# Performance work log

Hardware: AMD Instinct MI355X
Metric: run time of the kernel (lower is better)

Reference implementation:

```python
import jax, jax.numpy as jnp
import numpy as np

N_HEAD, M_DIM, K_DIM, V_DIM = 16, 1024, 64, 64
LN_EPS = 1e-5


def setup_inputs() -> dict:
    key = jax.random.key(0)
    ks = jax.random.split(key, 10)
    B, L = 4, 2048
    q = jax.random.normal(ks[0], (B, L, M_DIM), dtype=jnp.float32)
    k = jax.random.normal(ks[1], (B, L, M_DIM), dtype=jnp.float32)
    v = jax.random.normal(ks[2], (B, L, M_DIM), dtype=jnp.float32)
    s = 1.0 / np.sqrt(M_DIM)
    W_qs = jax.random.normal(ks[3], (M_DIM, N_HEAD * K_DIM), dtype=jnp.float32) * s
    W_ks = jax.random.normal(ks[4], (M_DIM, N_HEAD * K_DIM), dtype=jnp.float32) * s
    W_vs = jax.random.normal(ks[5], (M_DIM, N_HEAD * V_DIM), dtype=jnp.float32) * s
    fc_w = jax.random.normal(ks[6], (N_HEAD * V_DIM, M_DIM), dtype=jnp.float32) * (1.0 / np.sqrt(N_HEAD * V_DIM))
    fc_b = jnp.zeros((M_DIM,), dtype=jnp.float32)
    ln_g = jnp.ones((M_DIM,), dtype=jnp.float32)
    ln_b = jnp.zeros((M_DIM,), dtype=jnp.float32)
    return {"q": q, "k": k, "v": v, "W_qs": W_qs, "W_ks": W_ks, "W_vs": W_vs,
            "fc_w": fc_w, "fc_b": fc_b, "ln_g": ln_g, "ln_b": ln_b}


def reference(q, k, v, W_qs, W_ks, W_vs, fc_w, fc_b, ln_g, ln_b):
    B, Lq, _ = q.shape
    residual = q
    # project and split heads: [B, L, H, D]
    qh = (q @ W_qs).reshape(B, Lq, N_HEAD, K_DIM)
    kh = (k @ W_ks).reshape(B, k.shape[1], N_HEAD, K_DIM)
    vh = (v @ W_vs).reshape(B, v.shape[1], N_HEAD, V_DIM)
    temperature = np.power(K_DIM, 0.5).astype(np.float32)
    # attention scores [B, H, Lq, Lk]
    attn = jnp.einsum('bqhd,bkhd->bhqk', qh, kh) / temperature
    attn = jax.nn.softmax(attn, axis=-1)
    out = jnp.einsum('bhqk,bkhd->bqhd', attn, vh).reshape(B, Lq, N_HEAD * V_DIM)
    out = out @ fc_w + fc_b
    x = out + residual
    mu = jnp.mean(x, axis=-1, keepdims=True)
    var = jnp.mean(jnp.square(x - mu), axis=-1, keepdims=True)
    return (x - mu) * jax.lax.rsqrt(var + LN_EPS) * ln_g + ln_b
```

## Files before the change

### kernel.cpp

```cpp
#include <hip/hip_runtime.h>
#include <math.h>

#define NHEAD 16
#define MDIM  1024
#define KD    64
#define BATCH 4
#define SEQ   2048
#define MROWS (BATCH*SEQ)

using short8 = __attribute__((ext_vector_type(8))) short;
using f4     = __attribute__((ext_vector_type(4))) float;
using f16x   = __attribute__((ext_vector_type(16))) float;

__device__ inline short f2bf(float x) {
  union { float f; unsigned u; } v; v.f = x;
  unsigned r = v.u + 0x7fffu + ((v.u >> 16) & 1u);
  return (short)(r >> 16);
}

__device__ __forceinline__ float fast_exp2(float x) {
#if __has_builtin(__builtin_amdgcn_exp2f)
  return __builtin_amdgcn_exp2f(x);
#else
  return exp2f(x);
#endif
}

__device__ __forceinline__ int pack_bf16(float lo, float hi) {
#if __has_builtin(__builtin_amdgcn_cvt_pk_bf16_f32)
  auto t = __builtin_amdgcn_cvt_pk_bf16_f32(lo, hi);
  int r; __builtin_memcpy(&r, &t, 4); return r;
#else
  unsigned u0 = __float_as_uint(lo) + 0x8000u;
  unsigned u1 = __float_as_uint(hi) + 0x8000u;
  return (int)__builtin_amdgcn_perm(u1, u0, 0x07060302u);
#endif
}

__device__ __forceinline__ void g2l16(const void* g, void* l) {
  __builtin_amdgcn_global_load_lds((const __attribute__((address_space(1))) unsigned int*)g,
                                   (__attribute__((address_space(3))) unsigned int*)l, 16, 0, 0);
}

__global__ void wtrans_kernel(const float* __restrict__ w0, const float* __restrict__ w1,
                              const float* __restrict__ w2, const float* __restrict__ w3,
                              short* __restrict__ o0, short* __restrict__ o1,
                              short* __restrict__ o2, short* __restrict__ o3) {
  int z = blockIdx.z;
  const float* in = z == 0 ? w0 : (z == 1 ? w1 : (z == 2 ? w2 : w3));
  short* out = z == 0 ? o0 : (z == 1 ? o1 : (z == 2 ? o2 : o3));
  __shared__ float t[32][33];
  int bx = blockIdx.x * 32, by = blockIdx.y * 32;
  int tx = threadIdx.x, ty = threadIdx.y;
#pragma unroll
  for (int i = 0; i < 4; i++)
    t[ty + i * 8][tx] = in[(size_t)(by + ty + i * 8) * MDIM + bx + tx];
  __syncthreads();
#pragma unroll
  for (int i = 0; i < 4; i++)
    out[(size_t)(bx + ty + i * 8) * MDIM + by + tx] = f2bf(t[tx][ty + i * 8]);
}

__global__ void cvt_kernel(const float* __restrict__ q, const float* __restrict__ k,
                           const float* __restrict__ v, short* __restrict__ qb,
                           short* __restrict__ kb, short* __restrict__ vb) {
  const float* in = blockIdx.y == 0 ? q : (blockIdx.y == 1 ? k : v);
  short* out = blockIdx.y == 0 ? qb : (blockIdx.y == 1 ? kb : vb);
  size_t i = (size_t)blockIdx.x * 256 + threadIdx.x;
  float4 a = ((const float4*)in)[2 * i];
  float4 b = ((const float4*)in)[2 * i + 1];
  short8 s = {f2bf(a.x), f2bf(a.y), f2bf(a.z), f2bf(a.w),
              f2bf(b.x), f2bf(b.y), f2bf(b.z), f2bf(b.w)};
  ((short8*)out)[i] = s;
}

#define GEMM_STAGE_SETUP(Ab, Bt)                                                   \
  int srow = lane >> 2;                                                            \
  int sch = (lane & 3) ^ (srow & 3);                                               \
  const short* aSrc0 = Ab + (size_t)(m0 + wave * 32 + srow) * 1024 + sch * 8;      \
  const short* aSrc1 = aSrc0 + (size_t)16 * 1024;                                  \
  const short* bSrc0 = Bt + (size_t)(n0 + wave * 32 + srow) * 1024 + sch * 8;      \
  const short* bSrc1 = bSrc0 + (size_t)16 * 1024;

#define GEMM_MAIN_LOOP()                                                           \
  auto stage = [&](int k0, int b) {                                                \
    g2l16(aSrc0 + k0, &As[b][wave * 1024]);                                        \
    g2l16(aSrc1 + k0, &As[b][wave * 1024 + 512]);                                  \
    g2l16(bSrc0 + k0, &Bs[b][wave * 1024]);                                        \
    g2l16(bSrc1 + k0, &Bs[b][wave * 1024 + 512]);                                  \
  };                                                                               \
  stage(0, 0);                                                                     \
  __syncthreads();                                                                 \
  int aoff = (quad ^ (low & 3)) * 8;                                               \
  for (int k0 = 0; k0 < 1024; k0 += 32) {                                          \
    int b = (k0 >> 5) & 1;                                                         \
    if (k0 + 32 < 1024) stage(k0 + 32, b ^ 1);                                     \
    short8 af[4], bfr[4];                                                          \
    _Pragma("unroll")                                                              \
    for (int m = 0; m < 4; m++) af[m] = *(const short8*)&As[b][(wr + m * 16 + low) * 32 + aoff]; \
    _Pragma("unroll")                                                              \
    for (int n = 0; n < 4; n++) bfr[n] = *(const short8*)&Bs[b][(wc + n * 16 + low) * 32 + aoff]; \
    _Pragma("unroll")                                                              \
    for (int m = 0; m < 4; m++)                                                    \
      _Pragma("unroll")                                                            \
      for (int n = 0; n < 4; n++)                                                  \
        acc[m][n] = __builtin_amdgcn_mfma_f32_16x16x32_bf16(af[m], bfr[n], acc[m][n], 0, 0, 0); \
    __syncthreads();                                                               \
  }

__launch_bounds__(256, 4)
__global__ void gemm_qkv_kernel(const short* __restrict__ qb, const short* __restrict__ kb,
                                const short* __restrict__ vb, const short* __restrict__ Wqt,
                                const short* __restrict__ Wkt, const short* __restrict__ Wvt,
                                short* __restrict__ Qh, short* __restrict__ Kh,
                                short* __restrict__ Vt) {
  __shared__ __attribute__((aligned(16))) short As[2][128 * 32];
  __shared__ __attribute__((aligned(16))) short Bs[2][128 * 32];
  int z = blockIdx.z;
  const short* Ab = z == 0 ? qb : (z == 1 ? kb : vb);
  const short* Bt = z == 0 ? Wqt : (z == 1 ? Wkt : Wvt);
  int tid = threadIdx.x, wave = tid >> 6, lane = tid & 63;
  int quad = lane >> 4, low = lane & 15;
  int m0 = blockIdx.x * 128, n0 = blockIdx.y * 128;
  int wr = (wave >> 1) * 64, wc = (wave & 1) * 64;

  GEMM_STAGE_SETUP(Ab, Bt)

  f4 acc[4][4];
#pragma unroll
  for (int m = 0; m < 4; m++)
#pragma unroll
    for (int n = 0; n < 4; n++) { acc[m][n][0] = 0.f; acc[m][n][1] = 0.f; acc[m][n][2] = 0.f; acc[m][n][3] = 0.f; }

  GEMM_MAIN_LOOP()

  float scale = z == 0 ? 0.18033688011112042f : 1.0f;
  short* dst = z == 0 ? Qh : (z == 1 ? Kh : Vt);
#pragma unroll
  for (int m = 0; m < 4; m++)
#pragma unroll
    for (int n = 0; n < 4; n++)
#pragma unroll
      for (int r2 = 0; r2 < 4; r2++) {
        int gr = m0 + wr + m * 16 + quad * 4 + r2;
        int gc = n0 + wc + n * 16 + low;
        float val = acc[m][n][r2];
        int b = gr >> 11, l = gr & 2047, h = gc >> 6, d = gc & 63;
        if (z < 2)
          dst[(((size_t)(b * NHEAD + h)) * SEQ + l) * KD + d] = f2bf(val * scale);
        else
          dst[(((size_t)(b * NHEAD + h)) * KD + d) * SEQ + l] = f2bf(val);
      }
}

__launch_bounds__(256, 4)
__global__ void gemm_fc_kernel(const short* __restrict__ Ab, const short* __restrict__ Bt,
                               float* __restrict__ dst, const float* __restrict__ bias,
                               const float* __restrict__ res) {
  __shared__ __attribute__((aligned(16))) short As[2][128 * 32];
  __shared__ __attribute__((aligned(16))) short Bs[2][128 * 32];
  int tid = threadIdx.x, wave = tid >> 6, lane = tid & 63;
  int quad = lane >> 4, low = lane & 15;
  int m0 = blockIdx.x * 128, n0 = blockIdx.y * 128;
  int wr = (wave >> 1) * 64, wc = (wave & 1) * 64;

  GEMM_STAGE_SETUP(Ab, Bt)

  f4 acc[4][4];
#pragma unroll
  for (int m = 0; m < 4; m++)
#pragma unroll
    for (int n = 0; n < 4; n++) { acc[m][n][0] = 0.f; acc[m][n][1] = 0.f; acc[m][n][2] = 0.f; acc[m][n][3] = 0.f; }

  GEMM_MAIN_LOOP()

#pragma unroll
  for (int m = 0; m < 4; m++)
#pragma unroll
    for (int n = 0; n < 4; n++)
#pragma unroll
      for (int r2 = 0; r2 < 4; r2++) {
        int gr = m0 + wr + m * 16 + quad * 4 + r2;
        int gc = n0 + wc + n * 16 + low;
        dst[(size_t)gr * 1024 + gc] = acc[m][n][r2] + bias[gc] + res[(size_t)gr * 1024 + gc];
      }
}

__launch_bounds__(256, 4)
__global__ void attn_kernel(const short* __restrict__ Qh, const short* __restrict__ Kh,
                            const short* __restrict__ Vt, short* __restrict__ Out) {
  __shared__ __attribute__((aligned(16))) short KT[2][64 * 64];
  __shared__ __attribute__((aligned(16))) short VT[2][64 * 64];
  int tid = threadIdx.x;
  int wave = tid >> 6, lane = tid & 63;
  int l = lane & 31, hi = lane >> 5;
  int bh = blockIdx.y;
  int q0 = blockIdx.x * 128 + wave * 32;

  const short* Qb = Qh + (size_t)bh * SEQ * KD;
  const short* Kb = Kh + (size_t)bh * SEQ * KD;
  const short* Vb = Vt + (size_t)bh * KD * SEQ;

  int srow = lane >> 3;
  int sch = (lane & 7) ^ srow;
  const short* kSrc0 = Kb + (size_t)(wave * 16 + srow) * KD + sch * 8;
  const short* kSrc1 = kSrc0 + (size_t)8 * KD;
  const short* vSrc0 = Vb + (size_t)(wave * 16 + srow) * SEQ + sch * 8;
  const short* vSrc1 = vSrc0 + (size_t)8 * SEQ;

  auto stage = [&](int k0, int b) {
    g2l16(kSrc0 + (size_t)k0 * KD, &KT[b][wave * 1024]);
    g2l16(kSrc1 + (size_t)k0 * KD, &KT[b][wave * 1024 + 512]);
    g2l16(vSrc0 + k0, &VT[b][wave * 1024]);
    g2l16(vSrc1 + k0, &VT[b][wave * 1024 + 512]);
  };

  short8 qf[4];
#pragma unroll
  for (int ks = 0; ks < 4; ks++)
    qf[ks] = *(const short8*)&Qb[(size_t)(q0 + l) * KD + ks * 16 + hi * 8];

  f16x Oacc[2], lacc;
#pragma unroll
  for (int i = 0; i < 16; i++) { Oacc[0][i] = 0.f; Oacc[1][i] = 0.f; lacc[i] = 0.f; }
  const short8 onesb = {0x3F80, 0x3F80, 0x3F80, 0x3F80, 0x3F80, 0x3F80, 0x3F80, 0x3F80};

  stage(0, 0);
  __syncthreads();

  for (int c = 0; c < SEQ / 64; c++) {
    int b = c & 1;
    if (c + 1 < SEQ / 64) stage((c + 1) * 64, b ^ 1);

#pragma unroll
    for (int nt = 0; nt < 2; nt++) {
      short8 kf[4];
#pragma unroll
      for (int ks = 0; ks < 4; ks++)
        kf[ks] = *(const short8*)&KT[b][(nt * 32 + l) * 64 + (((ks * 2 + hi) ^ (l & 7)) * 8)];

      f16x S;
#pragma unroll
      for (int i = 0; i < 16; i++) S[i] = 0.f;
      __builtin_amdgcn_s_setprio(1);
#pragma unroll
      for (int ks = 0; ks < 4; ks++)
        S = __builtin_amdgcn_mfma_f32_32x32x16_bf16(kf[ks], qf[ks], S, 0, 0, 0);
      __builtin_amdgcn_s_setprio(0);

      int u[8];
#pragma unroll
      for (int i = 0; i < 8; i++)
        u[i] = pack_bf16(fast_exp2(S[2 * i]), fast_exp2(S[2 * i + 1]));
      asm("v_permlane32_swap_b32 %0, %1" : "+v"(u[0]), "+v"(u[2]));
      asm("v_permlane32_swap_b32 %0, %1" : "+v"(u[1]), "+v"(u[3]));
      asm("v_permlane32_swap_b32 %0, %1" : "+v"(u[4]), "+v"(u[6]));
      asm("v_permlane32_swap_b32 %0, %1" : "+v"(u[5]), "+v"(u[7]));
      short8 pa0, pa1;
      {
        int t0[4] = {u[0], u[1], u[2], u[3]};
        int t1[4] = {u[4], u[5], u[6], u[7]};
        __builtin_memcpy(&pa0, t0, 16);
        __builtin_memcpy(&pa1, t1, 16);
      }

      __builtin_amdgcn_s_setprio(1);
      lacc = __builtin_amdgcn_mfma_f32_32x32x16_bf16(pa0, onesb, lacc, 0, 0, 0);
      lacc = __builtin_amdgcn_mfma_f32_32x32x16_bf16(pa1, onesb, lacc, 0, 0, 0);

#pragma unroll
      for (int dt = 0; dt < 2; dt++) {
        short8 vf0 = *(const short8*)&VT[b][(dt * 32 + l) * 64 + (((nt * 4 + 0 + hi) ^ (l & 7)) * 8)];
        short8 vf1 = *(const short8*)&VT[b][(dt * 32 + l) * 64 + (((nt * 4 + 2 + hi) ^ (l & 7)) * 8)];
        Oacc[dt] = __builtin_amdgcn_mfma_f32_32x32x16_bf16(pa0, vf0, Oacc[dt], 0, 0, 0);
        Oacc[dt] = __builtin_amdgcn_mfma_f32_32x32x16_bf16(pa1, vf1, Oacc[dt], 0, 0, 0);
      }
      __builtin_amdgcn_s_setprio(0);
    }
    __syncthreads();
  }

  int bb = bh >> 4, h = bh & 15;
#pragma unroll
  for (int r = 0; r < 16; r++) {
    int qrow = q0 + (r & 3) + 8 * (r >> 2) + 4 * hi;
    float iv = 1.0f / lacc[r];
#pragma unroll
    for (int dt = 0; dt < 2; dt++) {
      size_t idx = ((size_t)(bb * SEQ + qrow)) * 1024 + h * 64 + dt * 32 + l;
      Out[idx] = f2bf(Oacc[dt][r] * iv);
    }
  }
}

__launch_bounds__(256)
__global__ void ln_kernel(const float* __restrict__ x, const float* __restrict__ g,
                          const float* __restrict__ b, float* __restrict__ out) {
  int row = blockIdx.x, tid = threadIdx.x;
  const float4* xr = (const float4*)(x + (size_t)row * 1024);
  float4 v = xr[tid];
  float s = v.x + v.y + v.z + v.w;
  float q = v.x * v.x + v.y * v.y + v.z * v.z + v.w * v.w;
#pragma unroll
  for (int o = 32; o > 0; o >>= 1) { s += __shfl_xor(s, o); q += __shfl_xor(q, o); }
  __shared__ float ss[4], sq[4];
  if ((tid & 63) == 0) { ss[tid >> 6] = s; sq[tid >> 6] = q; }
  __syncthreads();
  if (tid == 0) {
    float S = ss[0] + ss[1] + ss[2] + ss[3];
    float Q = sq[0] + sq[1] + sq[2] + sq[3];
    float mean = S * (1.f / 1024.f);
    float var = Q * (1.f / 1024.f) - mean * mean;
    ss[0] = mean; sq[0] = rsqrtf(var + 1e-5f);
  }
  __syncthreads();
  float mean = ss[0], rs = sq[0];
  const float4* g4 = (const float4*)g;
  const float4* b4 = (const float4*)b;
  float4 gg = g4[tid], bb = b4[tid], o;
  o.x = (v.x - mean) * rs * gg.x + bb.x;
  o.y = (v.y - mean) * rs * gg.y + bb.y;
  o.z = (v.z - mean) * rs * gg.z + bb.z;
  o.w = (v.w - mean) * rs * gg.w + bb.w;
  ((float4*)(out + (size_t)row * 1024))[tid] = o;
}

extern "C" void kernel_launch(void* const* d_in, const int* in_sizes, int n_in,
                              void* d_out, int out_size, void* d_ws, size_t ws_size,
                              hipStream_t stream) {
  const float* q   = (const float*)d_in[0];
  const float* k   = (const float*)d_in[1];
  const float* v   = (const float*)d_in[2];
  const float* Wq  = (const float*)d_in[3];
  const float* Wk  = (const float*)d_in[4];
  const float* Wv  = (const float*)d_in[5];
  const float* fcw = (const float*)d_in[6];
  const float* fcb = (const float*)d_in[7];
  const float* lng = (const float*)d_in[8];
  const float* lnb = (const float*)d_in[9];
  float* out = (float*)d_out;

  char* ws = (char*)d_ws;
  const size_t MB = 1024 * 1024;
  short* Wqt = (short*)(ws + 0 * MB);
  short* Wkt = (short*)(ws + 2 * MB);
  short* Wvt = (short*)(ws + 4 * MB);
  short* fct = (short*)(ws + 6 * MB);
  short* qb  = (short*)(ws + 8 * MB);
  short* kb  = (short*)(ws + 24 * MB);
  short* vb  = (short*)(ws + 40 * MB);
  short* Kh  = (short*)(ws + 8 * MB);
  short* Vt  = (short*)(ws + 24 * MB);
  short* Ao  = (short*)(ws + 40 * MB);
  short* Qh  = (short*)(ws + 56 * MB);
  float* X   = (float*)(ws + 8 * MB);

  wtrans_kernel<<<dim3(32, 32, 4), dim3(32, 8), 0, stream>>>(Wq, Wk, Wv, fcw, Wqt, Wkt, Wvt, fct);

  cvt_kernel<<<dim3(MROWS * MDIM / 8 / 256, 3), 256, 0, stream>>>(q, k, v, qb, kb, vb);

  gemm_qkv_kernel<<<dim3(64, 8, 3), 256, 0, stream>>>(qb, kb, vb, Wqt, Wkt, Wvt, Qh, Kh, Vt);

  attn_kernel<<<dim3(SEQ / 128, BATCH * NHEAD), 256, 0, stream>>>(Qh, Kh, Vt, Ao);

  gemm_fc_kernel<<<dim3(64, 8), 256, 0, stream>>>(Ao, fct, X, fcb, q);

  ln_kernel<<<MROWS, 256, 0, stream>>>(X, lng, lnb, out);
}
```

Before: 377.3 us.

## Rework bf16 GEMMs to 256x128 tiles, 8 waves, BK=64 with explicit waitcnt pipelining

Both the QKV projection and FC GEMMs now use 512-thread blocks computing 256x128 tiles with a K-step of 64 and a 2-deep LDS buffer. The first two stages are prefetched, and the loop waits with explicit vmcnt/lgkmcnt counters, scheduling fences, raw barriers and s_setprio around the MFMA burst. The goal is more reuse per LDS load and better overlap of global-to-LDS copies with MFMA work. LDS use per block grows to 96KB, which limits blocks per CU, and the grid halves, which may reduce load balance across CUs.

```diff
diff --git a/kernel.cpp b/kernel.cpp
--- a/kernel.cpp
+++ b/kernel.cpp
@@ -41,6 +41,12 @@
   __builtin_amdgcn_global_load_lds((const __attribute__((address_space(1))) unsigned int*)g,
                                    (__attribute__((address_space(3))) unsigned int*)l, 16, 0, 0);
 }
+
+#define AHIP_WAIT_LGKM0 asm volatile("s_waitcnt lgkmcnt(0)" ::: "memory")
+#define AHIP_WAIT_VM6   asm volatile("s_waitcnt vmcnt(6)" ::: "memory")
+#define AHIP_WAIT_VM0   asm volatile("s_waitcnt vmcnt(0)" ::: "memory")
+#define AHIP_SFENCE     __builtin_amdgcn_sched_barrier(0)
+#define AHIP_BAR        __builtin_amdgcn_s_barrier()
 
 __global__ void wtrans_kernel(const float* __restrict__ w0, const float* __restrict__ w1,
                               const float* __restrict__ w2, const float* __restrict__ w3,
@@ -74,77 +80,97 @@
   ((short8*)out)[i] = s;
 }
 
-#define GEMM_STAGE_SETUP(Ab, Bt)                                                   \
-  int srow = lane >> 2;                                                            \
-  int sch = (lane & 3) ^ (srow & 3);                                               \
-  const short* aSrc0 = Ab + (size_t)(m0 + wave * 32 + srow) * 1024 + sch * 8;      \
-  const short* aSrc1 = aSrc0 + (size_t)16 * 1024;                                  \
-  const short* bSrc0 = Bt + (size_t)(n0 + wave * 32 + srow) * 1024 + sch * 8;      \
-  const short* bSrc1 = bSrc0 + (size_t)16 * 1024;
-
-#define GEMM_MAIN_LOOP()                                                           \
-  auto stage = [&](int k0, int b) {                                                \
-    g2l16(aSrc0 + k0, &As[b][wave * 1024]);                                        \
-    g2l16(aSrc1 + k0, &As[b][wave * 1024 + 512]);                                  \
-    g2l16(bSrc0 + k0, &Bs[b][wave * 1024]);                                        \
-    g2l16(bSrc1 + k0, &Bs[b][wave * 1024 + 512]);                                  \
-  };                                                                               \
-  stage(0, 0);                                                                     \
-  __syncthreads();                                                                 \
-  int aoff = (quad ^ (low & 3)) * 8;                                               \
-  for (int k0 = 0; k0 < 1024; k0 += 32) {                                          \
-    int b = (k0 >> 5) & 1;                                                         \
-    if (k0 + 32 < 1024) stage(k0 + 32, b ^ 1);                                     \
-    short8 af[4], bfr[4];                                                          \
-    _Pragma("unroll")                                                              \
-    for (int m = 0; m < 4; m++) af[m] = *(const short8*)&As[b][(wr + m * 16 + low) * 32 + aoff]; \
-    _Pragma("unroll")                                                              \
-    for (int n = 0; n < 4; n++) bfr[n] = *(const short8*)&Bs[b][(wc + n * 16 + low) * 32 + aoff]; \
-    _Pragma("unroll")                                                              \
-    for (int m = 0; m < 4; m++)                                                    \
-      _Pragma("unroll")                                                            \
-      for (int n = 0; n < 4; n++)                                                  \
-        acc[m][n] = __builtin_amdgcn_mfma_f32_16x16x32_bf16(af[m], bfr[n], acc[m][n], 0, 0, 0); \
-    __syncthreads();                                                               \
+#define G8_PROLOGUE(Ab, Bt)                                                            \
+  int tid = threadIdx.x, wid = tid >> 6, lane = tid & 63;                              \
+  int quad = lane >> 4, low = lane & 15;                                               \
+  int l8 = lane & 7, lr = lane >> 3;                                                   \
+  int wrow = (wid >> 2) * 128, wcol = (wid & 3) * 32;                                  \
+  const short* aS = Ab + (size_t)(m0 + wid * 32 + lr) * 1024 + (l8 ^ lr) * 8;          \
+  const short* bS = Bt + (size_t)(n0 + wid * 16 + lr) * 1024 + (l8 ^ lr) * 8;          \
+  auto stage = [&](int t, int b) {                                                     \
+    const short* a = aS + t * 64;                                                      \
+    const short* bb = bS + t * 64;                                                     \
+    short* ad = &As[b][wid * 2048];                                                    \
+    short* bd = &Bs[b][wid * 1024];                                                    \
+    g2l16(a, ad);                                                                      \
+    g2l16(a + 8 * 1024, ad + 512);                                                     \
+    g2l16(a + 16 * 1024, ad + 1024);                                                   \
+    g2l16(a + 24 * 1024, ad + 1536);                                                   \
+    g2l16(bb, bd);                                                                     \
+    g2l16(bb + 8 * 1024, bd + 512);                                                    \
+  };                                                                                   \
+  f4 acc[8][2];                                                                        \
+  _Pragma("unroll")                                                                    \
+  for (int mf = 0; mf < 8; mf++)                                                       \
+    _Pragma("unroll")                                                                  \
+    for (int nf = 0; nf < 2; nf++) {                                                   \
+      acc[mf][nf][0] = 0.f; acc[mf][nf][1] = 0.f;                                      \
+      acc[mf][nf][2] = 0.f; acc[mf][nf][3] = 0.f;                                      \
+    }                                                                                  \
+  stage(0, 0);                                                                         \
+  stage(1, 1);                                                                         \
+  AHIP_WAIT_VM6; AHIP_SFENCE; AHIP_BAR; AHIP_SFENCE;
+
+#define G8_MAIN_LOOP()                                                                 \
+  for (int t = 0; t < 16; ++t) {                                                       \
+    const int cur = t & 1;                                                             \
+    short8 af[2][8], bfv[2][2];                                                        \
+    _Pragma("unroll")                                                                  \
+    for (int kk = 0; kk < 2; kk++) {                                                   \
+      _Pragma("unroll")                                                                \
+      for (int mf = 0; mf < 8; mf++)                                                   \
+        af[kk][mf] = *(const short8*)&As[cur][(wrow + mf * 16 + low) * 64 +            \
+                                              (((kk * 4 + quad) ^ (low & 7)) * 8)];    \
+      _Pragma("unroll")                                                                \
+      for (int nf = 0; nf < 2; nf++)                                                   \
+        bfv[kk][nf] = *(const short8*)&Bs[cur][(wcol + nf * 16 + low) * 64 +           \
+                                               (((kk * 4 + quad) ^ (low & 7)) * 8)];   \
+    }                                                                                  \
+    AHIP_WAIT_LGKM0; AHIP_SFENCE;                                                      \
+    AHIP_BAR; AHIP_SFENCE;                                                             \
+    if (t + 2 < 16) stage(t + 2, cur);                                                 \
+    __builtin_amdgcn_s_setprio(1);                                                     \
+    _Pragma("unroll")                                                                  \
+    for (int kk = 0; kk < 2; kk++)                                                     \
+      _Pragma("unroll")                                                                \
+      for (int mf = 0; mf < 8; mf++)                                                   \
+        _Pragma("unroll")                                                              \
+        for (int nf = 0; nf < 2; nf++)                                                 \
+          acc[mf][nf] = __builtin_amdgcn_mfma_f32_16x16x32_bf16(af[kk][mf],            \
+                          bfv[kk][nf], acc[mf][nf], 0, 0, 0);                          \
+    __builtin_amdgcn_s_setprio(0);                                                     \
+    AHIP_SFENCE;                                                                       \
+    if (t + 2 < 16) { AHIP_WAIT_VM6; } else { AHIP_WAIT_VM0; }                         \
+    AHIP_SFENCE; AHIP_BAR; AHIP_SFENCE;                                                \
   }
 
-__launch_bounds__(256, 4)
+__launch_bounds__(512, 2)
 __global__ void gemm_qkv_kernel(const short* __restrict__ qb, const short* __restrict__ kb,
                                 const short* __restrict__ vb, const short* __restrict__ Wqt,
                                 const short* __restrict__ Wkt, const short* __restrict__ Wvt,
                                 short* __restrict__ Qh, short* __restrict__ Kh,
                                 short* __restrict__ Vt) {
-  __shared__ __attribute__((aligned(16))) short As[2][128 * 32];
-  __shared__ __attribute__((aligned(16))) short Bs[2][128 * 32];
+  __shared__ __attribute__((aligned(16))) short As[2][256 * 64];
+  __shared__ __attribute__((aligned(16))) short Bs[2][128 * 64];
   int z = blockIdx.z;
   const short* Ab = z == 0 ? qb : (z == 1 ? kb : vb);
   const short* Bt = z == 0 ? Wqt : (z == 1 ? Wkt : Wvt);
-  int tid = threadIdx.x, wave = tid >> 6, lane = tid & 63;
-  int quad = lane >> 4, low = lane & 15;
-  int m0 = blockIdx.x * 128, n0 = blockIdx.y * 128;
-  int wr = (wave >> 1) * 64, wc = (wave & 1) * 64;
-
-  GEMM_STAGE_SETUP(Ab, Bt)
-
-  f4 acc[4][4];
-#pragma unroll
-  for (int m = 0; m < 4; m++)
-#pragma unroll
-    for (int n = 0; n < 4; n++) { acc[m][n][0] = 0.f; acc[m][n][1] = 0.f; acc[m][n][2] = 0.f; acc[m][n][3] = 0.f; }
-
-  GEMM_MAIN_LOOP()
+  int m0 = blockIdx.x * 256, n0 = blockIdx.y * 128;
+
+  G8_PROLOGUE(Ab, Bt)
+  G8_MAIN_LOOP()
 
   float scale = z == 0 ? 0.18033688011112042f : 1.0f;
   short* dst = z == 0 ? Qh : (z == 1 ? Kh : Vt);
 #pragma unroll
-  for (int m = 0; m < 4; m++)
-#pragma unroll
-    for (int n = 0; n < 4; n++)
+  for (int mf = 0; mf < 8; mf++)
+#pragma unroll
+    for (int nf = 0; nf < 2; nf++)
 #pragma unroll
       for (int r2 = 0; r2 < 4; r2++) {
-        int gr = m0 + wr + m * 16 + quad * 4 + r2;
-        int gc = n0 + wc + n * 16 + low;
-        float val = acc[m][n][r2];
+        int gr = m0 + wrow + mf * 16 + quad * 4 + r2;
+        int gc = n0 + wcol + nf * 16 + low;
+        float val = acc[mf][nf][r2];
         int b = gr >> 11, l = gr & 2047, h = gc >> 6, d = gc & 63;
         if (z < 2)
           dst[(((size_t)(b * NHEAD + h)) * SEQ + l) * KD + d] = f2bf(val * scale);
@@ -153,36 +179,26 @@
       }
 }
 
-__launch_bounds__(256, 4)
+__launch_bounds__(512, 2)
 __global__ void gemm_fc_kernel(const short* __restrict__ Ab, const short* __restrict__ Bt,
                                float* __restrict__ dst, const float* __restrict__ bias,
                                const float* __restrict__ res) {
-  __shared__ __attribute__((aligned(16))) short As[2][128 * 32];
-  __shared__ __attribute__((aligned(16))) short Bs[2][128 * 32];
-  int tid = threadIdx.x, wave = tid >> 6, lane = tid & 63;
-  int quad = lane >> 4, low = lane & 15;
-  int m0 = blockIdx.x * 128, n0 = blockIdx.y * 128;
-  int wr = (wave >> 1) * 64, wc = (wave & 1) * 64;
-
-  GEMM_STAGE_SETUP(Ab, Bt)
-
-  f4 acc[4][4];
-#pragma unroll
-  for (int m = 0; m < 4; m++)
-#pragma unroll
-    for (int n = 0; n < 4; n++) { acc[m][n][0] = 0.f; acc[m][n][1] = 0.f; acc[m][n][2] = 0.f; acc[m][n][3] = 0.f; }
-
-  GEMM_MAIN_LOOP()
-
-#pragma unroll
-  for (int m = 0; m < 4; m++)
-#pragma unroll
-    for (int n = 0; n < 4; n++)
+  __shared__ __attribute__((aligned(16))) short As[2][256 * 64];
+  __shared__ __attribute__((aligned(16))) short Bs[2][128 * 64];
+  int m0 = blockIdx.x * 256, n0 = blockIdx.y * 128;
+
+  G8_PROLOGUE(Ab, Bt)
+  G8_MAIN_LOOP()
+
+#pragma unroll
+  for (int mf = 0; mf < 8; mf++)
+#pragma unroll
+    for (int nf = 0; nf < 2; nf++)
 #pragma unroll
       for (int r2 = 0; r2 < 4; r2++) {
-        int gr = m0 + wr + m * 16 + quad * 4 + r2;
-        int gc = n0 + wc + n * 16 + low;
-        dst[(size_t)gr * 1024 + gc] = acc[m][n][r2] + bias[gc] + res[(size_t)gr * 1024 + gc];
+        int gr = m0 + wrow + mf * 16 + quad * 4 + r2;
+        int gc = n0 + wcol + nf * 16 + low;
+        dst[(size_t)gr * 1024 + gc] = acc[mf][nf][r2] + bias[gc] + res[(size_t)gr * 1024 + gc];
       }
 }
 
@@ -359,11 +375,11 @@
 
   cvt_kernel<<<dim3(MROWS * MDIM / 8 / 256, 3), 256, 0, stream>>>(q, k, v, qb, kb, vb);
 
-  gemm_qkv_kernel<<<dim3(64, 8, 3), 256, 0, stream>>>(qb, kb, vb, Wqt, Wkt, Wvt, Qh, Kh, Vt);
+  gemm_qkv_kernel<<<dim3(32, 8, 3), 512, 0, stream>>>(qb, kb, vb, Wqt, Wkt, Wvt, Qh, Kh, Vt);
 
   attn_kernel<<<dim3(SEQ / 128, BATCH * NHEAD), 256, 0, stream>>>(Qh, Kh, Vt, Ao);
 
-  gemm_fc_kernel<<<dim3(64, 8), 256, 0, stream>>>(Ao, fct, X, fcb, q);
+  gemm_fc_kernel<<<dim3(32, 8), 512, 0, stream>>>(Ao, fct, X, fcb, q);
 
   ln_kernel<<<MROWS, 256, 0, stream>>>(X, lng, lnb, out);
 }
```

Result: faster. 360.6 us (-4.4%).
